# Performance work log

Measured on AMD Instinct MI355X. Metric: run time of the kernel, lower is better.

Reference implementation:

```python
import jax, jax.numpy as jnp
import numpy as np

NEG_INF = -1e30

def dwconv1(x, dw, db, pw, pb):
    # DWConv with kernel_size=1: depthwise = per-channel scale+bias, pointwise = dense linear.
    # x: [B, L, H]
    return (x * dw + db) @ pw.T + pb

def masked_softmax(logits, maskf, axis):
    # masked_softmax as in SQuAD repos: mask*logits + (1-mask)*(-1e30), then softmax over axis
    m = maskf * logits + (1.0 - maskf) * NEG_INF
    return jax.nn.softmax(m, axis=axis)

def setup_inputs() -> dict:
    key = jax.random.key(0)
    ks = jax.random.split(key, 20)
    B, L, H = 4, 4096, 1024
    s = 1.0 / np.sqrt(H)
    inp = {
        "x": jax.random.normal(ks[0], (B, L, H), dtype=jnp.float32),
        "mask": jax.random.randint(ks[1], (B, L), 0, 2, dtype=jnp.int32),
    }
    names = ["k", "q", "v", "r"]
    for i, n in enumerate(names):
        inp[n + "_dw"] = jax.random.normal(ks[2 + 4 * i], (H,), dtype=jnp.float32) * 0.1 + 1.0
        inp[n + "_db"] = jnp.zeros((H,), dtype=jnp.float32)
        inp[n + "_pw"] = jax.random.normal(ks[3 + 4 * i], (H, H), dtype=jnp.float32) * s
        inp[n + "_pb"] = jnp.zeros((H,), dtype=jnp.float32)
    return inp

def reference(x, mask, k_dw, k_db, k_pw, k_pb, q_dw, q_db, q_pw, q_pb,
              v_dw, v_db, v_pw, v_pb, r_dw, r_db, r_pw, r_pb):
    B, L, H = x.shape
    n_head = 16
    hc = H // n_head
    maskf = mask.astype(x.dtype)[:, None, None, :]  # [B,1,1,L]

    def heads(t):  # [B,L,H] -> [B,nh,hc,L]
        return t.reshape(B, L, n_head, hc).transpose(0, 2, 3, 1)

    keys = heads(dwconv1(x, k_dw, k_db, k_pw, k_pb))
    queries = heads(dwconv1(x, q_dw, q_db, q_pw, q_pb))
    values = heads(dwconv1(x, v_dw, v_db, v_pw, v_pb))

    key_sm = masked_softmax(keys, maskf, axis=3)      # softmax over L
    query_sm = masked_softmax(queries, maskf, axis=2)  # softmax over head channels

    # context = key @ value^T : [B,nh,hc,hc]
    context = jnp.einsum("bhcl,bhdl->bhcd", key_sm, values)
    # attended = context^T @ query : [B,nh,hc(value),L]
    attended = jnp.einsum("bhcd,bhcl->bhdl", context, query_sm)

    agg = attended.transpose(0, 3, 1, 2).reshape(B, L, H)  # concat heads, [B,L,H]
    # dropout is identity in eval mode
    return dwconv1(agg, r_dw, r_db, r_pw, r_pb)
```

## Files before the change

kernel.cpp:

```cpp
#include <hip/hip_runtime.h>
#include <stdint.h>

#define H 1024
#define LSEQ 4096
#define NBATCH 4
#define MT (NBATCH*LSEQ)

typedef __attribute__((ext_vector_type(8))) short bf16x8;
typedef __attribute__((ext_vector_type(4))) short s16x4;
typedef __attribute__((ext_vector_type(4))) float f32x4;

static __device__ __forceinline__ unsigned short f2bf(float f){
  union { float f; unsigned u; } v; v.f = f;
  unsigned u = v.u;
  return (unsigned short)((u + 0x7FFFu + ((u >> 16) & 1u)) >> 16);
}
static __device__ __forceinline__ float bf2f(unsigned short h){
  union { unsigned u; float f; } v; v.u = ((unsigned)h) << 16;
  return v.f;
}
static __device__ __forceinline__ void g2l16(const void* g, void* l){
  __builtin_amdgcn_global_load_lds((const __attribute__((address_space(1))) void*)g,
                                   (__attribute__((address_space(3))) void*)l, 16, 0, 0);
}
static __device__ __forceinline__ f32x4 mfma16(bf16x8 a, bf16x8 b, f32x4 c){
  return __builtin_amdgcn_mfma_f32_16x16x32_bf16(a, b, c, 0, 0, 0);
}

struct P4 { const float* pw[4]; const float* dw[4]; const float* db[4]; const float* pb[4]; };

__global__ __launch_bounds__(256) void prepcvt(P4 a, const float* __restrict__ x,
    short* __restrict__ wb, float* __restrict__ bo, short* __restrict__ xb){
  const int bid = blockIdx.x, t = threadIdx.x;
  if (bid < 4096){
    __shared__ float red[256];
    const int p = bid >> 10, j = bid & 1023;
    const float* row = a.pw[p] + (size_t)j * H;
    const float* dwp = a.dw[p];
    const float* dbp = a.db[p];
    float acc = 0.f;
    #pragma unroll
    for (int k = 0; k < 4; ++k){
      int i = k*256 + t;
      float pv = row[i];
      wb[((size_t)p*H + j)*H + i] = (short)f2bf(pv * dwp[i]);
      acc += dbp[i] * pv;
    }
    red[t] = acc; __syncthreads();
    for (int s = 128; s > 0; s >>= 1){
      if (t < s) red[t] += red[t+s];
      __syncthreads();
    }
    if (t == 0) bo[p*H + j] = a.pb[p][j] + red[0];
  } else {
    const size_t base = ((size_t)(bid - 4096) * 4096) + (size_t)t * 16;
    #pragma unroll
    for (int h2 = 0; h2 < 2; ++h2){
      const float4* p = (const float4*)(x + base + h2*8);
      float4 u = p[0], v = p[1];
      bf16x8 o;
      o[0]=(short)f2bf(u.x); o[1]=(short)f2bf(u.y); o[2]=(short)f2bf(u.z); o[3]=(short)f2bf(u.w);
      o[4]=(short)f2bf(v.x); o[5]=(short)f2bf(v.y); o[6]=(short)f2bf(v.z); o[7]=(short)f2bf(v.w);
      *(bf16x8*)(xb + base + h2*8) = o;
    }
  }
}

template<int MODE, int NBLK>
__global__ __launch_bounds__(512, 2) void gemm8(const short* __restrict__ A,
    const short* __restrict__ WBp, const float* __restrict__ bia,
    short* __restrict__ oq, short* __restrict__ okT, short* __restrict__ ovT,
    float* __restrict__ ofin){
  __shared__ __align__(16) short lsm[2][2][256*64];

  const int nwg = NBLK * 64;
  const int cpx = nwg >> 3;
  const int bid = blockIdx.x;
  const int swz = (bid & 7) * cpx + (bid >> 3);
  const int mb = swz / NBLK, nb = swz % NBLK;
  const int m0 = mb * 256, n0 = nb * 256;

  const int tid  = threadIdx.x;
  const int lane = tid & 63;
  const int w    = tid >> 6;
  const int wm   = w >> 2, wn = w & 3;
  const int q4 = lane >> 4, r16 = lane & 15;
  const int rl = lane >> 3, sl = lane & 7;
  const int srcsw = ((sl ^ rl) << 3);

#define STAGE_A(BUF_, Q_, KB_) \
  g2l16(A + (size_t)(m0 + (Q_)*64 + w*8 + rl)*H + (KB_) + srcsw, \
        &lsm[0][BUF_][((Q_)*64 + w*8)*64])
#define STAGE_B(BUF_, Q_, KB_) \
  g2l16(WBp + (size_t)(n0 + (Q_)*64 + w*8 + rl)*H + (KB_) + srcsw, \
        &lsm[1][BUF_][((Q_)*64 + w*8)*64])
#define RD_A(dst, BUF_, MI8, KK) { const int row_ = wm*128 + (MI8)*16 + r16; \
  dst = *(const bf16x8*)&lsm[0][BUF_][row_*64 + ((((KK)*4+q4) ^ (row_&7))<<3)]; }
#define RD_B(dst, BUF_, NI4, KK) { const int row_ = wn*64 + (NI4)*16 + r16; \
  dst = *(const bf16x8*)&lsm[1][BUF_][row_*64 + ((((KK)*4+q4) ^ (row_&7))<<3)]; }

  f32x4 acc[8][4] = {};
  bf16x8 aF[4][2], bFa[2][2], bFb[2][2];

  STAGE_B(0,0,0); STAGE_B(0,1,0); STAGE_B(0,2,0); STAGE_B(0,3,0);
  STAGE_A(0,0,0); STAGE_A(0,2,0); STAGE_A(0,1,0); STAGE_A(0,3,0);
  asm volatile("s_waitcnt vmcnt(2)" ::: "memory");
  __builtin_amdgcn_s_barrier();

  #pragma unroll 2
  for (int t = 0; t < 16; ++t){
    const int buf = t & 1, sbuf = buf ^ 1;
    const int skb = ((t < 15) ? (t + 1) : 15) << 6;

    STAGE_B(sbuf, 0, skb); STAGE_B(sbuf, 1, skb);
    STAGE_B(sbuf, 2, skb); STAGE_B(sbuf, 3, skb);
    STAGE_A(sbuf, 0, skb); STAGE_A(sbuf, 2, skb);
    STAGE_A(sbuf, 1, skb); STAGE_A(sbuf, 3, skb);
    #pragma unroll
    for (int mi = 0; mi < 4; ++mi){ RD_A(aF[mi][0], buf, mi, 0); RD_A(aF[mi][1], buf, mi, 1); }
    #pragma unroll
    for (int ni = 0; ni < 2; ++ni){ RD_B(bFa[ni][0], buf, ni, 0); RD_B(bFa[ni][1], buf, ni, 1); }
    #pragma unroll
    for (int ni = 0; ni < 2; ++ni){ RD_B(bFb[ni][0], buf, 2+ni, 0); RD_B(bFb[ni][1], buf, 2+ni, 1); }
    __builtin_amdgcn_s_setprio(1);
    #pragma unroll
    for (int kk = 0; kk < 2; ++kk)
      #pragma unroll
      for (int mi = 0; mi < 4; ++mi){
        #pragma unroll
        for (int ni = 0; ni < 2; ++ni)
          acc[mi][ni] = mfma16(aF[mi][kk], bFa[ni][kk], acc[mi][ni]);
        #pragma unroll
        for (int ni = 0; ni < 2; ++ni)
          acc[mi][2+ni] = mfma16(aF[mi][kk], bFb[ni][kk], acc[mi][2+ni]);
      }
    __builtin_amdgcn_s_setprio(0);
    asm volatile("s_waitcnt vmcnt(8)" ::: "memory");
    __builtin_amdgcn_s_barrier();

    #pragma unroll
    for (int mi = 0; mi < 4; ++mi){ RD_A(aF[mi][0], buf, 4+mi, 0); RD_A(aF[mi][1], buf, 4+mi, 1); }
    __builtin_amdgcn_s_setprio(1);
    #pragma unroll
    for (int kk = 0; kk < 2; ++kk)
      #pragma unroll
      for (int mi = 0; mi < 4; ++mi){
        #pragma unroll
        for (int ni = 0; ni < 2; ++ni)
          acc[4+mi][ni] = mfma16(aF[mi][kk], bFa[ni][kk], acc[4+mi][ni]);
        #pragma unroll
        for (int ni = 0; ni < 2; ++ni)
          acc[4+mi][2+ni] = mfma16(aF[mi][kk], bFb[ni][kk], acc[4+mi][2+ni]);
      }
    __builtin_amdgcn_s_setprio(0);
    asm volatile("s_waitcnt vmcnt(2)" ::: "memory");
    __builtin_amdgcn_s_barrier();
  }
#undef STAGE_A
#undef STAGE_B
#undef RD_A
#undef RD_B

  if (MODE == 1){
    #pragma unroll
    for (int ni4 = 0; ni4 < 4; ++ni4){
      const int n = n0 + wn*64 + ni4*16 + r16;
      const float bv = bia[n];
      #pragma unroll
      for (int mi8 = 0; mi8 < 8; ++mi8){
        const int mbse = m0 + wm*128 + mi8*16 + q4*4;
        #pragma unroll
        for (int j = 0; j < 4; ++j)
          ofin[(size_t)(mbse+j)*H + n] = acc[mi8][ni4][j] + bv;
      }
    }
  } else {
    const int p = n0 >> 10;
    if (p == 1){
      #pragma unroll
      for (int ni4 = 0; ni4 < 4; ++ni4){
        const int n = n0 + wn*64 + ni4*16 + r16;
        const float bv = bia[n];
        const int ch = n & 1023;
        #pragma unroll
        for (int mi8 = 0; mi8 < 8; ++mi8){
          const int mbse = m0 + wm*128 + mi8*16 + q4*4;
          #pragma unroll
          for (int j = 0; j < 4; ++j)
            oq[(size_t)(mbse+j)*H + ch] = (short)f2bf(acc[mi8][ni4][j] + bv);
        }
      }
    } else {
      asm volatile("s_waitcnt vmcnt(0)" ::: "memory");
      __syncthreads();
      char* sC = (char*)&lsm[0][0][0];
      #pragma unroll
      for (int ni4 = 0; ni4 < 4; ++ni4){
        const int cr = wn*64 + ni4*16 + r16;
        const float bv = bia[n0 + cr];
        #pragma unroll
        for (int mi8 = 0; mi8 < 8; ++mi8){
          const int s8 = wm*32 + mi8*4 + q4;
          s16x4 v;
          #pragma unroll
          for (int j = 0; j < 4; ++j) v[j] = (short)f2bf(acc[mi8][ni4][j] + bv);
          *(s16x4*)(sC + cr*512 + ((s8 ^ ((cr & 7) << 1)) << 3)) = v;
        }
      }
      __syncthreads();
      short* ot = (p == 0) ? okT : ovT;
      const int ch0 = n0 & 1023, bb = m0 >> 12, lp0 = m0 & 4095;
      const int c = lane & 31;
      #pragma unroll
      for (int it = 0; it < 16; ++it){
        const int cr = it*16 + w*2 + (lane >> 5);
        bf16x8 vv = *(bf16x8*)(sC + cr*512 + ((c ^ (cr & 7)) << 4));
        *(bf16x8*)&ot[((size_t)bb*H + ch0 + cr)*LSEQ + lp0 + c*8] = vv;
      }
    }
  }
}

__global__ __launch_bounds__(512) void ctx_k(const short* __restrict__ kT,
    const short* __restrict__ vT, const int* __restrict__ mask,
    float* __restrict__ ctxP, float* __restrict__ mloc, float* __restrict__ dloc){
  const int lc = blockIdx.x, h = blockIdx.y, b = blockIdx.z;
  __shared__ __align__(16) short lK[2][64*64];
  __shared__ __align__(16) short lV[2][64*64];
  __shared__ float sMx[64];
  __shared__ float sDenP[8][64];
  __shared__ int sMkG[2][64];
  __shared__ float sAcc[64][65];
  const int tid = threadIdx.x, lane = tid & 63, w = tid >> 6;
  const int grp = w >> 2, wg = w & 3, tig = tid & 255;
  const short* kb = kT + (size_t)(b*16 + h)*64*LSEQ;
  const short* vb = vT + (size_t)(b*16 + h)*64*LSEQ;
  const int l0 = lc*512;

  int mk8[8];
  {
    const int* mp = mask + (size_t)b*LSEQ + l0;
    int4 a0 = *(const int4*)&mp[lane*8];
    int4 a1 = *(const int4*)&mp[lane*8+4];
    mk8[0]=a0.x; mk8[1]=a0.y; mk8[2]=a0.z; mk8[3]=a0.w;
    mk8[4]=a1.x; mk8[5]=a1.y; mk8[6]=a1.z; mk8[7]=a1.w;
  }
  #pragma unroll
  for (int c2 = 0; c2 < 8; ++c2){
    const int ch = w*8 + c2;
    const short* rp = kb + (size_t)ch*LSEQ + l0;
    bf16x8 v0 = *(const bf16x8*)&rp[lane*8];
    float mm = -1e30f;
    #pragma unroll
    for (int e = 0; e < 8; ++e) if (mk8[e]) mm = fmaxf(mm, bf2f((unsigned short)v0[e]));
    #pragma unroll
    for (int off = 32; off >= 1; off >>= 1) mm = fmaxf(mm, __shfl_xor(mm, off));
    if (lane == 0) sMx[ch] = mm;
  }

  f32x4 acc[4] = {};
  float dsum = 0.f;
  const int sl = lane & 7, rl = lane >> 3;
  const int lsw = ((sl ^ rl) << 3);
  __syncthreads();
  for (int kc2 = 0; kc2 < 4; ++kc2){
    const int kc = kc2*2 + grp;
    __syncthreads();
    const int lb = l0 + kc*64;
    #pragma unroll
    for (int c = 0; c < 2; ++c){
      const int r = (wg*2+c)*8 + rl;
      g2l16(kb + (size_t)r*LSEQ + lb + lsw, &lK[grp][(wg*2+c)*512]);
      g2l16(vb + (size_t)r*LSEQ + lb + lsw, &lV[grp][(wg*2+c)*512]);
    }
    if (tig < 64) sMkG[grp][tig] = mask[(size_t)b*LSEQ + lb + tig];
    __syncthreads();
    {
      const int row = lane;
      const float mxr = sMx[row];
      #pragma unroll
      for (int k2 = 0; k2 < 2; ++k2){
        const int slog = wg*2 + k2;
        const int sp = slog ^ (row & 7);
        bf16x8 v = *(bf16x8*)&lK[grp][row*64 + (sp<<3)];
        bf16x8 o;
        #pragma unroll
        for (int e=0;e<8;++e){
          const float f = bf2f((unsigned short)v[e]);
          const float we = sMkG[grp][slog*8+e] ? __expf(f - mxr) : 0.0f;
          dsum += we;
          o[e] = (short)f2bf(we);
        }
        *(bf16x8*)&lK[grp][row*64 + (sp<<3)] = o;
      }
    }
    __syncthreads();
    const int q4 = lane >> 4, r16 = lane & 15;
    #pragma unroll
    for (int kk = 0; kk < 2; ++kk){
      const int slog = kk*4 + q4;
      const int rowA = wg*16 + r16;
      bf16x8 a = *(bf16x8*)&lK[grp][rowA*64 + ((slog ^ (rowA & 7))<<3)];
      #pragma unroll
      for (int ni = 0; ni < 4; ++ni){
        const int rowB = ni*16 + r16;
        bf16x8 bv = *(bf16x8*)&lV[grp][rowB*64 + ((slog ^ (rowB & 7))<<3)];
        acc[ni] = mfma16(a, bv, acc[ni]);
      }
    }
  }
  const int q4 = lane >> 4, r16 = lane & 15;
  sDenP[w][lane] = dsum;
  if (grp == 0){
    #pragma unroll
    for (int ni=0;ni<4;++ni){
      const int d = ni*16 + r16;
      #pragma unroll
      for (int j=0;j<4;++j)
        sAcc[wg*16 + q4*4 + j][d] = acc[ni][j];
    }
  }
  __syncthreads();
  if (grp == 1){
    float* op = ctxP + (((size_t)(b*16 + h)*8 + lc) << 12);
    #pragma unroll
    for (int ni=0;ni<4;++ni){
      const int d = ni*16 + r16;
      #pragma unroll
      for (int j=0;j<4;++j){
        const int c = wg*16 + q4*4 + j;
        op[c*64 + d] = acc[ni][j] + sAcc[c][d];
      }
    }
  }
  if (tid < 64){
    const int idx = (((b*16 + h)*8 + lc) << 6) + tid;
    mloc[idx] = sMx[tid];
    float dv = 0.f;
    #pragma unroll
    for (int ww = 0; ww < 8; ++ww) dv += sDenP[ww][tid];
    dloc[idx] = dv;
  }
}

__global__ __launch_bounds__(512) void attd_k(const short* __restrict__ qb,
    const float* __restrict__ ctxP, const float* __restrict__ mloc,
    const float* __restrict__ dloc, const int* __restrict__ mask,
    short* __restrict__ agg){
  const int lcb = blockIdx.x, h = blockIdx.y, b = blockIdx.z;
  __shared__ __align__(16) short lQ[2][64*64];
  __shared__ __align__(16) short lCt[64*64];
  __shared__ float sSc[8][64];
  const int tid = threadIdx.x, lane = tid & 63, w = tid >> 6;
  const int grp = w >> 2, wg = w & 3;
  if (tid < 64){
    const int base = ((b*16 + h) << 9) + tid;
    float m[8], e[8];
    #pragma unroll
    for (int i = 0; i < 8; ++i) m[i] = mloc[base + i*64];
    float mg = m[0];
    #pragma unroll
    for (int i = 1; i < 8; ++i) mg = fmaxf(mg, m[i]);
    float den = 0.f;
    #pragma unroll
    for (int i = 0; i < 8; ++i){ e[i] = __expf(m[i]-mg); den += e[i]*dloc[base + i*64]; }
    float inv = 1.0f / fmaxf(den, 1e-30f);
    #pragma unroll
    for (int i = 0; i < 8; ++i) sSc[i][tid] = e[i]*inv;
  }
  __syncthreads();
  {
    const int d = lane;
    const float* base = ctxP + ((size_t)(b*16 + h)*8 << 12);
    #pragma unroll
    for (int i=0;i<8;++i){
      const int c = w*8 + i;
      float s = 0.f;
      #pragma unroll
      for (int ch = 0; ch < 8; ++ch)
        s += base[ch*4096 + c*64 + d] * sSc[ch][c];
      lCt[d*64 + ((((c>>3) ^ (d&7))<<3) | (c&7))] = (short)f2bf(s);
    }
  }
  const int l0g = b*LSEQ + lcb*1024 + grp*512;
  const int sl = lane & 7, rl = lane >> 3;
  const int lsw = ((sl ^ rl) << 3);
  for (int sc = 0; sc < 8; ++sc){
    __syncthreads();
    #pragma unroll
    for (int c = 0; c < 2; ++c){
      const int r = (wg*2+c)*8 + rl;
      g2l16(qb + (size_t)(l0g + sc*64 + r)*H + h*64 + lsw, &lQ[grp][(wg*2+c)*512]);
    }
    __syncthreads();
    {
      const int row = wg*16 + (lane & 15);
      const int q4 = lane >> 4;
      const int mk = mask[(size_t)l0g + sc*64 + row];
      float vals[16];
      float mxv = -3e38f;
      #pragma unroll
      for (int k2=0;k2<2;++k2){
        const int slog = q4*2 + k2;
        const int sp = slog ^ (row & 7);
        bf16x8 v = *(bf16x8*)&lQ[grp][row*64 + (sp<<3)];
        #pragma unroll
        for (int e=0;e<8;++e){
          const float f = bf2f((unsigned short)v[e]);
          vals[k2*8+e] = f;
          mxv = fmaxf(mxv, f);
        }
      }
      mxv = fmaxf(mxv, __shfl_xor(mxv, 16));
      mxv = fmaxf(mxv, __shfl_xor(mxv, 32));
      float s = 0.f;
      #pragma unroll
      for (int e=0;e<16;++e){ vals[e] = __expf(vals[e]-mxv); s += vals[e]; }
      s += __shfl_xor(s, 16);
      s += __shfl_xor(s, 32);
      const float inv = 1.0f / s;
      #pragma unroll
      for (int k2=0;k2<2;++k2){
        const int slog = q4*2 + k2;
        const int sp = slog ^ (row & 7);
        bf16x8 o;
        #pragma unroll
        for (int e=0;e<8;++e)
          o[e] = (short)f2bf(mk ? vals[k2*8+e]*inv : 0.015625f);
        *(bf16x8*)&lQ[grp][row*64 + (sp<<3)] = o;
      }
    }
    __syncthreads();
    f32x4 acc[4] = {};
    const int q4 = lane >> 4, r16 = lane & 15;
    #pragma unroll
    for (int kk=0;kk<2;++kk){
      const int slog = kk*4 + q4;
      const int rowA = wg*16 + r16;
      bf16x8 a = *(bf16x8*)&lQ[grp][rowA*64 + ((slog ^ (rowA&7))<<3)];
      #pragma unroll
      for (int ni=0;ni<4;++ni){
        const int rowB = ni*16 + r16;
        bf16x8 bv = *(bf16x8*)&lCt[rowB*64 + ((slog ^ (rowB&7))<<3)];
        acc[ni] = mfma16(a, bv, acc[ni]);
      }
    }
    #pragma unroll
    for (int ni=0;ni<4;++ni){
      const int d = ni*16 + r16;
      #pragma unroll
      for (int j=0;j<4;++j){
        const int lrow = wg*16 + q4*4 + j;
        agg[(size_t)(l0g + sc*64 + lrow)*H + h*64 + d] = (short)f2bf(acc[ni][j]);
      }
    }
  }
}

extern "C" void kernel_launch(void* const* d_in, const int* in_sizes, int n_in,
                              void* d_out, int out_size, void* d_ws, size_t ws_size,
                              hipStream_t stream){
  (void)in_sizes; (void)n_in; (void)out_size; (void)ws_size;
  const float* x    = (const float*)d_in[0];
  const int*   mask = (const int*)d_in[1];
  P4 prm;
  for (int p2 = 0; p2 < 4; ++p2){
    prm.dw[p2] = (const float*)d_in[2 + 4*p2];
    prm.db[p2] = (const float*)d_in[3 + 4*p2];
    prm.pw[p2] = (const float*)d_in[4 + 4*p2];
    prm.pb[p2] = (const float*)d_in[5 + 4*p2];
  }
  char* ws = (char*)d_ws;
  short* WB   = (short*)(ws);
  float* BIAS = (float*)(ws + ((size_t)8<<20));
  float* MLOC = (float*)(ws + ((size_t)8<<20) + (256<<10));
  float* DLOC = (float*)(ws + ((size_t)8<<20) + (512<<10));
  short* XB   = (short*)(ws + ((size_t)9<<20));
  short* QB   = (short*)(ws + ((size_t)41<<20));
  short* KT   = (short*)(ws + ((size_t)73<<20));
  short* VT   = (short*)(ws + ((size_t)105<<20));
  float* CTXP = (float*)(ws + ((size_t)137<<20));
  short* AGG  = XB;

  prepcvt<<<8192, 256, 0, stream>>>(prm, x, WB, BIAS, XB);
  gemm8<0,12><<<768, 512, 0, stream>>>(XB, WB, BIAS, QB, KT, VT, nullptr);
  ctx_k<<<dim3(8,16,4), 512, 0, stream>>>(KT, VT, mask, CTXP, MLOC, DLOC);
  attd_k<<<dim3(4,16,4), 512, 0, stream>>>(QB, CTXP, MLOC, DLOC, mask, AGG);
  gemm8<1,4><<<256, 512, 0, stream>>>(AGG, WB + (size_t)3*H*H, BIAS + 3*1024,
                                      nullptr, nullptr, nullptr, (float*)d_out);
}
```

Baseline: 211.3 us.

## Halve GEMM K-tile to 32, template M-tile, use 128-row tiles for output GEMM

The GEMM kernel now stages K in chunks of 32 instead of 64, which halves shared memory to 64KB. It also drops the split two-phase inner loop and makes the M tile size a template parameter. The final projection GEMM uses 128-row tiles, launching 512 blocks instead of 256 to fill more CUs. The transposed epilogue is staged through the smaller shared buffer in two halves. The cost is twice as many barriers per K and a full vmcnt(0) wait each iteration, which reduces load/compute overlap.

```diff
diff --git a/kernel.cpp b/kernel.cpp
--- a/kernel.cpp
+++ b/kernel.cpp
@@ -66,94 +66,73 @@
   }
 }
 
-template<int MODE, int NBLK>
-__global__ __launch_bounds__(512, 2) void gemm8(const short* __restrict__ A,
+template<int MODE, int BM, int NBLK>
+__global__ __launch_bounds__(512, 2) void gemmk(const short* __restrict__ A,
     const short* __restrict__ WBp, const float* __restrict__ bia,
     short* __restrict__ oq, short* __restrict__ okT, short* __restrict__ ovT,
     float* __restrict__ ofin){
-  __shared__ __align__(16) short lsm[2][2][256*64];
-
-  const int nwg = NBLK * 64;
+  __shared__ __align__(16) short lsm[4][8192];
+
+  constexpr int MI = BM/32;
+  constexpr int MBLK = MT/BM;
+  const int nwg = NBLK * MBLK;
   const int cpx = nwg >> 3;
   const int bid = blockIdx.x;
   const int swz = (bid & 7) * cpx + (bid >> 3);
   const int mb = swz / NBLK, nb = swz % NBLK;
-  const int m0 = mb * 256, n0 = nb * 256;
+  const int m0 = mb * BM, n0 = nb * 256;
 
   const int tid  = threadIdx.x;
   const int lane = tid & 63;
   const int w    = tid >> 6;
   const int wm   = w >> 2, wn = w & 3;
   const int q4 = lane >> 4, r16 = lane & 15;
-  const int rl = lane >> 3, sl = lane & 7;
-  const int srcsw = ((sl ^ rl) << 3);
+  const int rl4 = lane >> 2;
+  const int srcsw = (((lane & 3) ^ ((lane >> 3) & 3)) << 3);
 
 #define STAGE_A(BUF_, Q_, KB_) \
-  g2l16(A + (size_t)(m0 + (Q_)*64 + w*8 + rl)*H + (KB_) + srcsw, \
-        &lsm[0][BUF_][((Q_)*64 + w*8)*64])
+  g2l16(A + (size_t)(m0 + (Q_)*128 + w*16 + rl4)*H + (KB_) + srcsw, \
+        &lsm[BUF_][((Q_)*128 + w*16)*32])
 #define STAGE_B(BUF_, Q_, KB_) \
-  g2l16(WBp + (size_t)(n0 + (Q_)*64 + w*8 + rl)*H + (KB_) + srcsw, \
-        &lsm[1][BUF_][((Q_)*64 + w*8)*64])
-#define RD_A(dst, BUF_, MI8, KK) { const int row_ = wm*128 + (MI8)*16 + r16; \
-  dst = *(const bf16x8*)&lsm[0][BUF_][row_*64 + ((((KK)*4+q4) ^ (row_&7))<<3)]; }
-#define RD_B(dst, BUF_, NI4, KK) { const int row_ = wn*64 + (NI4)*16 + r16; \
-  dst = *(const bf16x8*)&lsm[1][BUF_][row_*64 + ((((KK)*4+q4) ^ (row_&7))<<3)]; }
-
-  f32x4 acc[8][4] = {};
-  bf16x8 aF[4][2], bFa[2][2], bFb[2][2];
-
-  STAGE_B(0,0,0); STAGE_B(0,1,0); STAGE_B(0,2,0); STAGE_B(0,3,0);
-  STAGE_A(0,0,0); STAGE_A(0,2,0); STAGE_A(0,1,0); STAGE_A(0,3,0);
-  asm volatile("s_waitcnt vmcnt(2)" ::: "memory");
+  g2l16(WBp + (size_t)(n0 + (Q_)*128 + w*16 + rl4)*H + (KB_) + srcsw, \
+        &lsm[2+(BUF_)][((Q_)*128 + w*16)*32])
+#define RD_A(dst, BUF_, MIi) { const int row_ = wm*(BM/2) + (MIi)*16 + r16; \
+  dst = *(const bf16x8*)&lsm[BUF_][row_*32 + ((q4 ^ ((row_>>1)&3))<<3)]; }
+#define RD_B(dst, BUF_, NIi) { const int row_ = wn*64 + (NIi)*16 + r16; \
+  dst = *(const bf16x8*)&lsm[2+(BUF_)][row_*32 + ((q4 ^ ((row_>>1)&3))<<3)]; }
+
+  f32x4 acc[MI][4] = {};
+
+  STAGE_B(0,0,0); STAGE_B(0,1,0);
+  STAGE_A(0,0,0);
+  if constexpr (BM == 256) STAGE_A(0,1,0);
+  asm volatile("s_waitcnt vmcnt(0)" ::: "memory");
   __builtin_amdgcn_s_barrier();
 
   #pragma unroll 2
-  for (int t = 0; t < 16; ++t){
+  for (int t = 0; t < 32; ++t){
     const int buf = t & 1, sbuf = buf ^ 1;
-    const int skb = ((t < 15) ? (t + 1) : 15) << 6;
+    const int skb = ((t < 31) ? (t + 1) : 31) << 5;
 
     STAGE_B(sbuf, 0, skb); STAGE_B(sbuf, 1, skb);
-    STAGE_B(sbuf, 2, skb); STAGE_B(sbuf, 3, skb);
-    STAGE_A(sbuf, 0, skb); STAGE_A(sbuf, 2, skb);
-    STAGE_A(sbuf, 1, skb); STAGE_A(sbuf, 3, skb);
-    #pragma unroll
-    for (int mi = 0; mi < 4; ++mi){ RD_A(aF[mi][0], buf, mi, 0); RD_A(aF[mi][1], buf, mi, 1); }
-    #pragma unroll
-    for (int ni = 0; ni < 2; ++ni){ RD_B(bFa[ni][0], buf, ni, 0); RD_B(bFa[ni][1], buf, ni, 1); }
-    #pragma unroll
-    for (int ni = 0; ni < 2; ++ni){ RD_B(bFb[ni][0], buf, 2+ni, 0); RD_B(bFb[ni][1], buf, 2+ni, 1); }
+    STAGE_A(sbuf, 0, skb);
+    if constexpr (BM == 256) STAGE_A(sbuf, 1, skb);
+
+    bf16x8 aF[MI], bF[4];
+    #pragma unroll
+    for (int mi = 0; mi < MI; ++mi) RD_A(aF[mi], buf, mi);
+    #pragma unroll
+    for (int ni = 0; ni < 4; ++ni)  RD_B(bF[ni], buf, ni);
+
     __builtin_amdgcn_s_setprio(1);
     #pragma unroll
-    for (int kk = 0; kk < 2; ++kk)
-      #pragma unroll
-      for (int mi = 0; mi < 4; ++mi){
-        #pragma unroll
-        for (int ni = 0; ni < 2; ++ni)
-          acc[mi][ni] = mfma16(aF[mi][kk], bFa[ni][kk], acc[mi][ni]);
-        #pragma unroll
-        for (int ni = 0; ni < 2; ++ni)
-          acc[mi][2+ni] = mfma16(aF[mi][kk], bFb[ni][kk], acc[mi][2+ni]);
-      }
+    for (int mi = 0; mi < MI; ++mi)
+      #pragma unroll
+      for (int ni = 0; ni < 4; ++ni)
+        acc[mi][ni] = mfma16(aF[mi], bF[ni], acc[mi][ni]);
     __builtin_amdgcn_s_setprio(0);
-    asm volatile("s_waitcnt vmcnt(8)" ::: "memory");
-    __builtin_amdgcn_s_barrier();
-
-    #pragma unroll
-    for (int mi = 0; mi < 4; ++mi){ RD_A(aF[mi][0], buf, 4+mi, 0); RD_A(aF[mi][1], buf, 4+mi, 1); }
-    __builtin_amdgcn_s_setprio(1);
-    #pragma unroll
-    for (int kk = 0; kk < 2; ++kk)
-      #pragma unroll
-      for (int mi = 0; mi < 4; ++mi){
-        #pragma unroll
-        for (int ni = 0; ni < 2; ++ni)
-          acc[4+mi][ni] = mfma16(aF[mi][kk], bFa[ni][kk], acc[4+mi][ni]);
-        #pragma unroll
-        for (int ni = 0; ni < 2; ++ni)
-          acc[4+mi][2+ni] = mfma16(aF[mi][kk], bFb[ni][kk], acc[4+mi][2+ni]);
-      }
-    __builtin_amdgcn_s_setprio(0);
-    asm volatile("s_waitcnt vmcnt(2)" ::: "memory");
+
+    asm volatile("s_waitcnt vmcnt(0)" ::: "memory");
     __builtin_amdgcn_s_barrier();
   }
 #undef STAGE_A
@@ -167,8 +146,8 @@
       const int n = n0 + wn*64 + ni4*16 + r16;
       const float bv = bia[n];
       #pragma unroll
-      for (int mi8 = 0; mi8 < 8; ++mi8){
-        const int mbse = m0 + wm*128 + mi8*16 + q4*4;
+      for (int mi8 = 0; mi8 < MI; ++mi8){
+        const int mbse = m0 + wm*(BM/2) + mi8*16 + q4*4;
         #pragma unroll
         for (int j = 0; j < 4; ++j)
           ofin[(size_t)(mbse+j)*H + n] = acc[mi8][ni4][j] + bv;
@@ -183,39 +162,47 @@
         const float bv = bia[n];
         const int ch = n & 1023;
         #pragma unroll
-        for (int mi8 = 0; mi8 < 8; ++mi8){
-          const int mbse = m0 + wm*128 + mi8*16 + q4*4;
+        for (int mi8 = 0; mi8 < MI; ++mi8){
+          const int mbse = m0 + wm*(BM/2) + mi8*16 + q4*4;
           #pragma unroll
           for (int j = 0; j < 4; ++j)
             oq[(size_t)(mbse+j)*H + ch] = (short)f2bf(acc[mi8][ni4][j] + bv);
         }
       }
     } else {
-      asm volatile("s_waitcnt vmcnt(0)" ::: "memory");
-      __syncthreads();
-      char* sC = (char*)&lsm[0][0][0];
-      #pragma unroll
-      for (int ni4 = 0; ni4 < 4; ++ni4){
-        const int cr = wn*64 + ni4*16 + r16;
-        const float bv = bia[n0 + cr];
-        #pragma unroll
-        for (int mi8 = 0; mi8 < 8; ++mi8){
-          const int s8 = wm*32 + mi8*4 + q4;
-          s16x4 v;
-          #pragma unroll
-          for (int j = 0; j < 4; ++j) v[j] = (short)f2bf(acc[mi8][ni4][j] + bv);
-          *(s16x4*)(sC + cr*512 + ((s8 ^ ((cr & 7) << 1)) << 3)) = v;
-        }
-      }
-      __syncthreads();
       short* ot = (p == 0) ? okT : ovT;
+      char* sC = (char*)&lsm[0][0];
       const int ch0 = n0 & 1023, bb = m0 >> 12, lp0 = m0 & 4095;
       const int c = lane & 31;
-      #pragma unroll
-      for (int it = 0; it < 16; ++it){
-        const int cr = it*16 + w*2 + (lane >> 5);
-        bf16x8 vv = *(bf16x8*)(sC + cr*512 + ((c ^ (cr & 7)) << 4));
-        *(bf16x8*)&ot[((size_t)bb*H + ch0 + cr)*LSEQ + lp0 + c*8] = vv;
+      const int hpw = wn >> 1;
+      #pragma unroll
+      for (int hp = 0; hp < 2; ++hp){
+        if (hpw == hp){
+          #pragma unroll
+          for (int ni4 = 0; ni4 < 4; ++ni4){
+            const int cr = wn*64 + ni4*16 + r16;
+            const int crl = cr & 127;
+            const float bv = bia[n0 + cr];
+            #pragma unroll
+            for (int mi8 = 0; mi8 < MI; ++mi8){
+              const int s8 = wm*32 + mi8*4 + q4;
+              s16x4 v;
+              #pragma unroll
+              for (int j = 0; j < 4; ++j) v[j] = (short)f2bf(acc[mi8][ni4][j] + bv);
+              *(s16x4*)(sC + crl*512 + ((s8 ^ ((cr & 7) << 1)) << 3)) = v;
+            }
+          }
+        }
+        __syncthreads();
+        #pragma unroll
+        for (int i = 0; i < 8; ++i){
+          const int it = hp*8 + i;
+          const int cr = it*16 + w*2 + (lane >> 5);
+          const int crl = cr & 127;
+          bf16x8 vv = *(bf16x8*)(sC + crl*512 + ((c ^ (cr & 7)) << 4));
+          *(bf16x8*)&ot[((size_t)bb*H + ch0 + cr)*LSEQ + lp0 + c*8] = vv;
+        }
+        __syncthreads();
       }
     }
   }
@@ -483,9 +470,9 @@
   short* AGG  = XB;
 
   prepcvt<<<8192, 256, 0, stream>>>(prm, x, WB, BIAS, XB);
-  gemm8<0,12><<<768, 512, 0, stream>>>(XB, WB, BIAS, QB, KT, VT, nullptr);
+  gemmk<0,256,12><<<768, 512, 0, stream>>>(XB, WB, BIAS, QB, KT, VT, nullptr);
   ctx_k<<<dim3(8,16,4), 512, 0, stream>>>(KT, VT, mask, CTXP, MLOC, DLOC);
   attd_k<<<dim3(4,16,4), 512, 0, stream>>>(QB, CTXP, MLOC, DLOC, mask, AGG);
-  gemm8<1,4><<<256, 512, 0, stream>>>(AGG, WB + (size_t)3*H*H, BIAS + 3*1024,
-                                      nullptr, nullptr, nullptr, (float*)d_out);
-}
+  gemmk<1,128,4><<<512, 512, 0, stream>>>(AGG, WB + (size_t)3*H*H, BIAS + 3*1024,
+                                          nullptr, nullptr, nullptr, (float*)d_out);
+}
```

Result: slower. 220.9 us (+4.6%).
